# Kernel optimization log

Measured on AMD Instinct MI355X. Metric: run time of the kernel, lower is better.

Reference implementation:

```python
import jax, jax.numpy as jnp
import numpy as np

B, M, D, W = 4, 4096, 64, 128  # batch/heads, seq (m=n), head dim (k), nnz per row


def setup_inputs() -> dict:
    key = jax.random.key(0)
    kq, kk, kv, kc = jax.random.split(key, 4)
    q = jax.random.normal(kq, (B, M, D), dtype=jnp.float32)
    k = jax.random.normal(kk, (B, M, D), dtype=jnp.float32)
    v = jax.random.normal(kv, (B, M, D), dtype=jnp.float32)
    # CSR with uniform W nonzeros per row: row_offsets = arange(M+1)*W implicit,
    # column_indices flattened is [M*W]; stored here as [M, W].
    column_indices = jax.random.randint(kc, (M, W), 0, M).astype(jnp.int32)
    return {"q": q, "k": k, "v": v, "column_indices": column_indices}


def reference(q, k, v, column_indices):
    # SDDMM: logits[b,i,w] = <q[b,i,:], k[b, col[i,w], :]> at sparse positions only
    k_g = k[:, column_indices, :]                      # [B, M, W, D]
    logits = jnp.einsum('bmd,bmwd->bmw', q, k_g)       # sparse values per row
    # Sparse row-wise softmax (each CSR row has exactly W entries)
    weights = jax.nn.softmax(logits, axis=-1)          # [B, M, W]
    # SpMM: out[b,i,d] = sum_w weights[b,i,w] * v[b, col[i,w], d]
    v_g = v[:, column_indices, :]                      # [B, M, W, D]
    out = jnp.einsum('bmw,bmwd->bmd', weights, v_g)    # [B, M, D]
    return out
```

## Files before the change

### kernel.cpp

```cpp
#include <hip/hip_runtime.h>
#include <hip/hip_fp16.h>
#include <math.h>

constexpr int B = 4;
constexpr int M = 4096;
constexpr int D = 64;
constexpr int W = 128;
constexpr int NELEM = B * M * D;

typedef _Float16 h2_t __attribute__((ext_vector_type(2)));
typedef int      i4_t __attribute__((ext_vector_type(4)));

__global__ __launch_bounds__(256) void cvt_f32_f16_2(
    const float4* __restrict__ k, const float4* __restrict__ v,
    __half2* __restrict__ kh, __half2* __restrict__ vh, int n4) {
    int i = blockIdx.x * 256 + threadIdx.x;
    const float4* src;
    __half2* dst;
    if (i < n4) { src = k; dst = kh; }
    else        { src = v; dst = vh; i -= n4; if (i >= n4) return; }
    float4 f = src[i];
    dst[2 * i]     = __floats2half2_rn(f.x, f.y);
    dst[2 * i + 1] = __floats2half2_rn(f.z, f.w);
}

__global__ __launch_bounds__(256, 4) void sparse_attn_f16(
    const float* __restrict__ q,
    const __half* __restrict__ kh,
    const __half* __restrict__ vh,
    const int*   __restrict__ idx,
    float*       __restrict__ out)
{
    const int blk  = blockIdx.x;
    const int b    = blk & 3;
    const int mb   = (blk >> 2) * 4;
    const int t    = threadIdx.x;
    const int wave = t >> 6;
    const int lane = t & 63;
    const int ci   = lane & 7;
    const int r    = lane >> 3;
    const int m    = mb + wave;

    __shared__ int idx_s[4 * W];

    ((int2*)idx_s)[t] = ((const int2*)(idx + (size_t)mb * W))[t];

    const float* qrow = q + ((size_t)b * M + m) * D;
    const float4 qa = ((const float4*)qrow)[2 * ci];
    const float4 qb = ((const float4*)qrow)[2 * ci + 1];
    h2_t qh[4];
    qh[0] = (h2_t){(_Float16)qa.x, (_Float16)qa.y};
    qh[1] = (h2_t){(_Float16)qa.z, (_Float16)qa.w};
    qh[2] = (h2_t){(_Float16)qb.x, (_Float16)qb.y};
    qh[3] = (h2_t){(_Float16)qb.z, (_Float16)qb.w};

    __syncthreads();

    int voff[16];
    #pragma unroll
    for (int j = 0; j < 16; ++j)
        voff[j] = idx_s[wave * W + j * 8 + r] * (D * 2) + ci * 16;

    const char* kb = (const char*)(kh + (size_t)b * M * D);
    const char* vb = (const char*)(vh + (size_t)b * M * D);

    float larr[16];
    #pragma unroll
    for (int batch = 0; batch < 2; ++batch) {
        i4_t kreg[8];
        #pragma unroll
        for (int jj = 0; jj < 8; ++jj)
            kreg[jj] = __builtin_nontemporal_load(
                (const i4_t*)(kb + voff[batch * 8 + jj]));
        #pragma unroll
        for (int jj = 0; jj < 8; ++jj) {
            union { i4_t v; h2_t h[4]; } u;
            u.v = kreg[jj];
            float part = 0.f;
            part = __builtin_amdgcn_fdot2(u.h[0], qh[0], part, false);
            part = __builtin_amdgcn_fdot2(u.h[1], qh[1], part, false);
            part = __builtin_amdgcn_fdot2(u.h[2], qh[2], part, false);
            part = __builtin_amdgcn_fdot2(u.h[3], qh[3], part, false);
            part += __shfl_xor(part, 1);
            part += __shfl_xor(part, 2);
            part += __shfl_xor(part, 4);
            larr[batch * 8 + jj] = part;
        }
    }

    i4_t vreg0[8];
    #pragma unroll
    for (int jj = 0; jj < 8; ++jj)
        vreg0[jj] = __builtin_nontemporal_load((const i4_t*)(vb + voff[jj]));

    float mx = larr[0];
    #pragma unroll
    for (int j = 1; j < 16; ++j) mx = fmaxf(mx, larr[j]);
    mx = fmaxf(mx, __shfl_xor(mx, 8));
    mx = fmaxf(mx, __shfl_xor(mx, 16));
    mx = fmaxf(mx, __shfl_xor(mx, 32));

    float sum = 0.f;
    #pragma unroll
    for (int j = 0; j < 16; ++j) { larr[j] = __expf(larr[j] - mx); sum += larr[j]; }
    sum += __shfl_xor(sum, 8);
    sum += __shfl_xor(sum, 16);
    sum += __shfl_xor(sum, 32);
    const float inv = 1.0f / sum;

    float acc[8] = {0, 0, 0, 0, 0, 0, 0, 0};
    i4_t vreg1[8];
    #pragma unroll
    for (int jj = 0; jj < 8; ++jj)
        vreg1[jj] = __builtin_nontemporal_load((const i4_t*)(vb + voff[8 + jj]));

    #pragma unroll
    for (int jj = 0; jj < 8; ++jj) {
        const float p = larr[jj];
        union { i4_t v; h2_t h[4]; } u;
        u.v = vreg0[jj];
        #pragma unroll
        for (int c = 0; c < 4; ++c) {
            acc[2 * c]     += p * (float)u.h[c][0];
            acc[2 * c + 1] += p * (float)u.h[c][1];
        }
    }
    #pragma unroll
    for (int jj = 0; jj < 8; ++jj) {
        const float p = larr[8 + jj];
        union { i4_t v; h2_t h[4]; } u;
        u.v = vreg1[jj];
        #pragma unroll
        for (int c = 0; c < 4; ++c) {
            acc[2 * c]     += p * (float)u.h[c][0];
            acc[2 * c + 1] += p * (float)u.h[c][1];
        }
    }
    #pragma unroll
    for (int o = 8; o < 64; o <<= 1) {
        #pragma unroll
        for (int i = 0; i < 8; ++i) acc[i] += __shfl_xor(acc[i], o);
    }

    if (r == 0) {
        float4* orow = (float4*)(out + ((size_t)b * M + m) * D);
        orow[2 * ci]     = make_float4(acc[0] * inv, acc[1] * inv,
                                       acc[2] * inv, acc[3] * inv);
        orow[2 * ci + 1] = make_float4(acc[4] * inv, acc[5] * inv,
                                       acc[6] * inv, acc[7] * inv);
    }
}

__global__ __launch_bounds__(128) void sparse_attn_f32(
    const float* __restrict__ q,
    const float* __restrict__ k,
    const float* __restrict__ v,
    const int*   __restrict__ idx,
    float*       __restrict__ out)
{
    const int blk = blockIdx.x;
    const int b = blk & 3;
    const int m = blk >> 2;
    const int t = threadIdx.x;
    const int lane = t & 63;
    const int wave = t >> 6;
    const int ci = lane & 15;
    const int r  = lane >> 4;

    __shared__ int   idx_s[W];
    __shared__ float sc_s[W];
    __shared__ float red_s[4];
    __shared__ float4 opart_s[16];

    idx_s[t] = idx[m * W + t];
    const float4 qf = ((const float4*)(q + ((size_t)b * M + m) * D))[ci];
    __syncthreads();

    const float* kb = k + (size_t)b * M * D;
    const int wbase = wave * 64;

    #pragma unroll
    for (int j = 0; j < 16; ++j) {
        const int w = wbase + j * 4 + r;
        const float4 kv = ((const float4*)(kb + (size_t)idx_s[w] * D))[ci];
        float part = kv.x * qf.x + kv.y * qf.y + kv.z * qf.z + kv.w * qf.w;
        part += __shfl_xor(part, 1);
        part += __shfl_xor(part, 2);
        part += __shfl_xor(part, 4);
        part += __shfl_xor(part, 8);
        if (ci == 0) sc_s[w] = part;
    }
    __syncthreads();

    float logit = sc_s[t];
    float mx = logit;
    #pragma unroll
    for (int o = 1; o < 64; o <<= 1) mx = fmaxf(mx, __shfl_xor(mx, o));
    if (lane == 0) red_s[wave] = mx;
    __syncthreads();
    mx = fmaxf(red_s[0], red_s[1]);
    float e = __expf(logit - mx);
    float sm = e;
    #pragma unroll
    for (int o = 1; o < 64; o <<= 1) sm += __shfl_xor(sm, o);
    if (lane == 0) red_s[2 + wave] = sm;
    __syncthreads();
    const float inv_denom = 1.0f / (red_s[2] + red_s[3]);
    sc_s[t] = e * inv_denom;
    __syncthreads();

    const float* vb = v + (size_t)b * M * D;
    float4 acc = {0.f, 0.f, 0.f, 0.f};
    #pragma unroll
    for (int j = 0; j < 16; ++j) {
        const int w = wbase + j * 4 + r;
        const float p = sc_s[w];
        const float4 vv = ((const float4*)(vb + (size_t)idx_s[w] * D))[ci];
        acc.x += p * vv.x; acc.y += p * vv.y;
        acc.z += p * vv.z; acc.w += p * vv.w;
    }
    acc.x += __shfl_xor(acc.x, 16); acc.y += __shfl_xor(acc.y, 16);
    acc.z += __shfl_xor(acc.z, 16); acc.w += __shfl_xor(acc.w, 16);
    acc.x += __shfl_xor(acc.x, 32); acc.y += __shfl_xor(acc.y, 32);
    acc.z += __shfl_xor(acc.z, 32); acc.w += __shfl_xor(acc.w, 32);

    if (wave == 0 && r == 0) opart_s[ci] = acc;
    __syncthreads();
    if (wave == 1 && r == 0) {
        const float4 o0 = opart_s[ci];
        float4 res;
        res.x = o0.x + acc.x; res.y = o0.y + acc.y;
        res.z = o0.z + acc.z; res.w = o0.w + acc.w;
        ((float4*)(out + ((size_t)b * M + m) * D))[ci] = res;
    }
}

extern "C" void kernel_launch(void* const* d_in, const int* in_sizes, int n_in,
                              void* d_out, int out_size, void* d_ws, size_t ws_size,
                              hipStream_t stream) {
    const float* q = (const float*)d_in[0];
    const float* k = (const float*)d_in[1];
    const float* v = (const float*)d_in[2];
    const int* idx = (const int*)d_in[3];
    float* out = (float*)d_out;

    const size_t need = (size_t)2 * NELEM * sizeof(__half);
    if (ws_size >= need) {
        __half* kh = (__half*)d_ws;
        __half* vh = kh + NELEM;
        const int n4 = NELEM / 4;
        const int cblk = (2 * n4 + 255) / 256;
        cvt_f32_f16_2<<<cblk, 256, 0, stream>>>((const float4*)k, (const float4*)v,
                                                (__half2*)kh, (__half2*)vh, n4);
        sparse_attn_f16<<<B * M / 4, 256, 0, stream>>>(q, kh, vh, idx, out);
    } else {
        sparse_attn_f32<<<B * M, 128, 0, stream>>>(q, k, v, idx, out);
    }
}
```

Before: 93.72 us.

## Spill logits to LDS and shrink load batches to raise occupancy

The fp16 sparse attention kernel now writes logits and exp weights to shared memory instead of holding 16 logits and 16 V vectors in registers. K and V gathers are issued in smaller batches of 4, and launch bounds are raised to 8 blocks per CU to get more waves in flight for latency hiding. The cost is fewer outstanding loads per wave, extra LDS traffic and two extra block barriers. V loads also no longer overlap with the softmax.

```diff
diff --git a/kernel.cpp b/kernel.cpp
--- a/kernel.cpp
+++ b/kernel.cpp
@@ -24,7 +24,7 @@
     dst[2 * i + 1] = __floats2half2_rn(f.z, f.w);
 }
 
-__global__ __launch_bounds__(256, 4) void sparse_attn_f16(
+__global__ __launch_bounds__(256, 8) void sparse_attn_f16(
     const float* __restrict__ q,
     const __half* __restrict__ kh,
     const __half* __restrict__ vh,
@@ -41,7 +41,8 @@
     const int r    = lane >> 3;
     const int m    = mb + wave;
 
-    __shared__ int idx_s[4 * W];
+    __shared__ int   idx_s[4 * W];
+    __shared__ float sc_s[4 * W];
 
     ((int2*)idx_s)[t] = ((const int2*)(idx + (size_t)mb * W))[t];
 
@@ -56,24 +57,23 @@
 
     __syncthreads();
 
-    int voff[16];
-    #pragma unroll
-    for (int j = 0; j < 16; ++j)
-        voff[j] = idx_s[wave * W + j * 8 + r] * (D * 2) + ci * 16;
-
     const char* kb = (const char*)(kh + (size_t)b * M * D);
     const char* vb = (const char*)(vh + (size_t)b * M * D);
-
-    float larr[16];
-    #pragma unroll
-    for (int batch = 0; batch < 2; ++batch) {
-        i4_t kreg[8];
-        #pragma unroll
-        for (int jj = 0; jj < 8; ++jj)
-            kreg[jj] = __builtin_nontemporal_load(
-                (const i4_t*)(kb + voff[batch * 8 + jj]));
-        #pragma unroll
-        for (int jj = 0; jj < 8; ++jj) {
+    const int wrow = wave * W;
+
+    float mx = -1e30f;
+    #pragma unroll
+    for (int batch = 0; batch < 4; ++batch) {
+        int voff[4];
+        #pragma unroll
+        for (int jj = 0; jj < 4; ++jj)
+            voff[jj] = idx_s[wrow + (batch * 4 + jj) * 8 + r] * (D * 2) + ci * 16;
+        i4_t kreg[4];
+        #pragma unroll
+        for (int jj = 0; jj < 4; ++jj)
+            kreg[jj] = __builtin_nontemporal_load((const i4_t*)(kb + voff[jj]));
+        #pragma unroll
+        for (int jj = 0; jj < 4; ++jj) {
             union { i4_t v; h2_t h[4]; } u;
             u.v = kreg[jj];
             float part = 0.f;
@@ -84,56 +84,51 @@
             part += __shfl_xor(part, 1);
             part += __shfl_xor(part, 2);
             part += __shfl_xor(part, 4);
-            larr[batch * 8 + jj] = part;
+            if (ci == 0) sc_s[wrow + (batch * 4 + jj) * 8 + r] = part;
+            mx = fmaxf(mx, part);
         }
     }
-
-    i4_t vreg0[8];
-    #pragma unroll
-    for (int jj = 0; jj < 8; ++jj)
-        vreg0[jj] = __builtin_nontemporal_load((const i4_t*)(vb + voff[jj]));
-
-    float mx = larr[0];
-    #pragma unroll
-    for (int j = 1; j < 16; ++j) mx = fmaxf(mx, larr[j]);
     mx = fmaxf(mx, __shfl_xor(mx, 8));
     mx = fmaxf(mx, __shfl_xor(mx, 16));
     mx = fmaxf(mx, __shfl_xor(mx, 32));
 
-    float sum = 0.f;
-    #pragma unroll
-    for (int j = 0; j < 16; ++j) { larr[j] = __expf(larr[j] - mx); sum += larr[j]; }
-    sum += __shfl_xor(sum, 8);
-    sum += __shfl_xor(sum, 16);
-    sum += __shfl_xor(sum, 32);
+    __syncthreads();
+
+    float e0 = __expf(sc_s[wrow + lane] - mx);
+    float e1 = __expf(sc_s[wrow + 64 + lane] - mx);
+    float sum = e0 + e1;
+    #pragma unroll
+    for (int o = 1; o < 64; o <<= 1) sum += __shfl_xor(sum, o);
     const float inv = 1.0f / sum;
+    sc_s[wrow + lane]      = e0;
+    sc_s[wrow + 64 + lane] = e1;
+
+    __syncthreads();
 
     float acc[8] = {0, 0, 0, 0, 0, 0, 0, 0};
-    i4_t vreg1[8];
-    #pragma unroll
-    for (int jj = 0; jj < 8; ++jj)
-        vreg1[jj] = __builtin_nontemporal_load((const i4_t*)(vb + voff[8 + jj]));
-
-    #pragma unroll
-    for (int jj = 0; jj < 8; ++jj) {
-        const float p = larr[jj];
-        union { i4_t v; h2_t h[4]; } u;
-        u.v = vreg0[jj];
-        #pragma unroll
-        for (int c = 0; c < 4; ++c) {
-            acc[2 * c]     += p * (float)u.h[c][0];
-            acc[2 * c + 1] += p * (float)u.h[c][1];
+    #pragma unroll
+    for (int batch = 0; batch < 4; ++batch) {
+        int voff[4];
+        float p[4];
+        #pragma unroll
+        for (int jj = 0; jj < 4; ++jj) {
+            const int w = (batch * 4 + jj) * 8 + r;
+            voff[jj] = idx_s[wrow + w] * (D * 2) + ci * 16;
+            p[jj] = sc_s[wrow + w];
         }
-    }
-    #pragma unroll
-    for (int jj = 0; jj < 8; ++jj) {
-        const float p = larr[8 + jj];
-        union { i4_t v; h2_t h[4]; } u;
-        u.v = vreg1[jj];
-        #pragma unroll
-        for (int c = 0; c < 4; ++c) {
-            acc[2 * c]     += p * (float)u.h[c][0];
-            acc[2 * c + 1] += p * (float)u.h[c][1];
+        i4_t vreg[4];
+        #pragma unroll
+        for (int jj = 0; jj < 4; ++jj)
+            vreg[jj] = __builtin_nontemporal_load((const i4_t*)(vb + voff[jj]));
+        #pragma unroll
+        for (int jj = 0; jj < 4; ++jj) {
+            union { i4_t v; h2_t h[4]; } u;
+            u.v = vreg[jj];
+            #pragma unroll
+            for (int c = 0; c < 4; ++c) {
+                acc[2 * c]     += p[jj] * (float)u.h[c][0];
+                acc[2 * c + 1] += p[jj] * (float)u.h[c][1];
+            }
         }
     }
     #pragma unroll
```

Result: slower. 106.9 us (+14.1%).

## Interleave fp16 K and V rows and fuse SDDMM, softmax and SpMM in one pass

Applied to the files above, without the earlier changes.

The conversion kernel now writes K and V as fp16 into one interleaved 256-byte row per key: K in the first 128 bytes, V in the second. In the attention kernel, each 16-lane group fetches K and V for the same gathered index in a single contiguous load. Lanes 0-7 compute the dot product, and lanes 8-15 receive the logit by shuffle and accumulate exp(logit)*V directly. The separate max pass and the second V gather phase are gone, which shortens the dependent-latency chain and merges two scattered accesses per index into one. In exchange, half the lanes do wasted arithmetic. Dropping max subtraction also risks fp32 overflow if logits grow large.

```diff
diff --git a/kernel.cpp b/kernel.cpp
--- a/kernel.cpp
+++ b/kernel.cpp
@@ -7,27 +7,35 @@
 constexpr int D = 64;
 constexpr int W = 128;
 constexpr int NELEM = B * M * D;
+constexpr int ROWB  = 256;
 
 typedef _Float16 h2_t __attribute__((ext_vector_type(2)));
 typedef int      i4_t __attribute__((ext_vector_type(4)));
 
-__global__ __launch_bounds__(256) void cvt_f32_f16_2(
+__global__ __launch_bounds__(256) void cvt_interleave(
     const float4* __restrict__ k, const float4* __restrict__ v,
-    __half2* __restrict__ kh, __half2* __restrict__ vh, int n4) {
-    int i = blockIdx.x * 256 + threadIdx.x;
+    char* __restrict__ ws) {
+    const int half = B * M * 8;
+    int id = blockIdx.x * 256 + threadIdx.x;
     const float4* src;
-    __half2* dst;
-    if (i < n4) { src = k; dst = kh; }
-    else        { src = v; dst = vh; i -= n4; if (i >= n4) return; }
-    float4 f = src[i];
-    dst[2 * i]     = __floats2half2_rn(f.x, f.y);
-    dst[2 * i + 1] = __floats2half2_rn(f.z, f.w);
-}
-
-__global__ __launch_bounds__(256, 4) void sparse_attn_f16(
+    int base;
+    if (id < half) { src = k; base = 0; }
+    else           { src = v; base = 128; id -= half; if (id >= half) return; }
+    const int row = id >> 3;
+    const int cc  = id & 7;
+    float4 f0 = src[row * 16 + cc * 2];
+    float4 f1 = src[row * 16 + cc * 2 + 1];
+    union { __half2 h[4]; i4_t v4; } u;
+    u.h[0] = __floats2half2_rn(f0.x, f0.y);
+    u.h[1] = __floats2half2_rn(f0.z, f0.w);
+    u.h[2] = __floats2half2_rn(f1.x, f1.y);
+    u.h[3] = __floats2half2_rn(f1.z, f1.w);
+    *(i4_t*)(ws + (size_t)row * ROWB + base + cc * 16) = u.v4;
+}
+
+__global__ __launch_bounds__(256, 4) void sparse_attn_ilv(
     const float* __restrict__ q,
-    const __half* __restrict__ kh,
-    const __half* __restrict__ vh,
+    const char*  __restrict__ ws,
     const int*   __restrict__ idx,
     float*       __restrict__ out)
 {
@@ -37,17 +45,17 @@
     const int t    = threadIdx.x;
     const int wave = t >> 6;
     const int lane = t & 63;
-    const int ci   = lane & 7;
-    const int r    = lane >> 3;
+    const int rg   = lane >> 4;
+    const int c    = lane & 15;
+    const int kc   = c & 7;
     const int m    = mb + wave;
 
     __shared__ int idx_s[4 * W];
-
     ((int2*)idx_s)[t] = ((const int2*)(idx + (size_t)mb * W))[t];
 
     const float* qrow = q + ((size_t)b * M + m) * D;
-    const float4 qa = ((const float4*)qrow)[2 * ci];
-    const float4 qb = ((const float4*)qrow)[2 * ci + 1];
+    const float4 qa = ((const float4*)qrow)[2 * kc];
+    const float4 qb = ((const float4*)qrow)[2 * kc + 1];
     h2_t qh[4];
     qh[0] = (h2_t){(_Float16)qa.x, (_Float16)qa.y};
     qh[1] = (h2_t){(_Float16)qa.z, (_Float16)qa.w};
@@ -56,26 +64,26 @@
 
     __syncthreads();
 
-    int voff[16];
-    #pragma unroll
-    for (int j = 0; j < 16; ++j)
-        voff[j] = idx_s[wave * W + j * 8 + r] * (D * 2) + ci * 16;
-
-    const char* kb = (const char*)(kh + (size_t)b * M * D);
-    const char* vb = (const char*)(vh + (size_t)b * M * D);
-
-    float larr[16];
-    #pragma unroll
-    for (int batch = 0; batch < 2; ++batch) {
-        i4_t kreg[8];
+    const char* plane = ws + (size_t)b * M * ROWB;
+    const int wrow = wave * W;
+
+    float2 acc[4] = {{0,0},{0,0},{0,0},{0,0}};
+    float sum = 0.f;
+
+    #pragma unroll
+    for (int batch = 0; batch < 4; ++batch) {
+        int voff[8];
         #pragma unroll
         for (int jj = 0; jj < 8; ++jj)
-            kreg[jj] = __builtin_nontemporal_load(
-                (const i4_t*)(kb + voff[batch * 8 + jj]));
+            voff[jj] = idx_s[wrow + (batch * 8 + jj) * 4 + rg] * ROWB + c * 16;
+        i4_t reg[8];
+        #pragma unroll
+        for (int jj = 0; jj < 8; ++jj)
+            reg[jj] = __builtin_nontemporal_load((const i4_t*)(plane + voff[jj]));
         #pragma unroll
         for (int jj = 0; jj < 8; ++jj) {
             union { i4_t v; h2_t h[4]; } u;
-            u.v = kreg[jj];
+            u.v = reg[jj];
             float part = 0.f;
             part = __builtin_amdgcn_fdot2(u.h[0], qh[0], part, false);
             part = __builtin_amdgcn_fdot2(u.h[1], qh[1], part, false);
@@ -84,70 +92,39 @@
             part += __shfl_xor(part, 1);
             part += __shfl_xor(part, 2);
             part += __shfl_xor(part, 4);
-            larr[batch * 8 + jj] = part;
+            const float recv  = __shfl_xor(part, 8);
+            const float logit = (c < 8) ? part : recv;
+            const float e = __expf(logit);
+            sum += e;
+            float2 f0 = __half22float2(*(const __half2*)&u.h[0]);
+            float2 f1 = __half22float2(*(const __half2*)&u.h[1]);
+            float2 f2 = __half22float2(*(const __half2*)&u.h[2]);
+            float2 f3 = __half22float2(*(const __half2*)&u.h[3]);
+            acc[0].x += e * f0.x; acc[0].y += e * f0.y;
+            acc[1].x += e * f1.x; acc[1].y += e * f1.y;
+            acc[2].x += e * f2.x; acc[2].y += e * f2.y;
+            acc[3].x += e * f3.x; acc[3].y += e * f3.y;
         }
     }
 
-    i4_t vreg0[8];
-    #pragma unroll
-    for (int jj = 0; jj < 8; ++jj)
-        vreg0[jj] = __builtin_nontemporal_load((const i4_t*)(vb + voff[jj]));
-
-    float mx = larr[0];
-    #pragma unroll
-    for (int j = 1; j < 16; ++j) mx = fmaxf(mx, larr[j]);
-    mx = fmaxf(mx, __shfl_xor(mx, 8));
-    mx = fmaxf(mx, __shfl_xor(mx, 16));
-    mx = fmaxf(mx, __shfl_xor(mx, 32));
-
-    float sum = 0.f;
-    #pragma unroll
-    for (int j = 0; j < 16; ++j) { larr[j] = __expf(larr[j] - mx); sum += larr[j]; }
-    sum += __shfl_xor(sum, 8);
-    sum += __shfl_xor(sum, 16);
-    sum += __shfl_xor(sum, 32);
+    #pragma unroll
+    for (int o = 16; o < 64; o <<= 1) {
+        sum += __shfl_xor(sum, o);
+        #pragma unroll
+        for (int i = 0; i < 4; ++i) {
+            acc[i].x += __shfl_xor(acc[i].x, o);
+            acc[i].y += __shfl_xor(acc[i].y, o);
+        }
+    }
     const float inv = 1.0f / sum;
 
-    float acc[8] = {0, 0, 0, 0, 0, 0, 0, 0};
-    i4_t vreg1[8];
-    #pragma unroll
-    for (int jj = 0; jj < 8; ++jj)
-        vreg1[jj] = __builtin_nontemporal_load((const i4_t*)(vb + voff[8 + jj]));
-
-    #pragma unroll
-    for (int jj = 0; jj < 8; ++jj) {
-        const float p = larr[jj];
-        union { i4_t v; h2_t h[4]; } u;
-        u.v = vreg0[jj];
-        #pragma unroll
-        for (int c = 0; c < 4; ++c) {
-            acc[2 * c]     += p * (float)u.h[c][0];
-            acc[2 * c + 1] += p * (float)u.h[c][1];
-        }
-    }
-    #pragma unroll
-    for (int jj = 0; jj < 8; ++jj) {
-        const float p = larr[8 + jj];
-        union { i4_t v; h2_t h[4]; } u;
-        u.v = vreg1[jj];
-        #pragma unroll
-        for (int c = 0; c < 4; ++c) {
-            acc[2 * c]     += p * (float)u.h[c][0];
-            acc[2 * c + 1] += p * (float)u.h[c][1];
-        }
-    }
-    #pragma unroll
-    for (int o = 8; o < 64; o <<= 1) {
-        #pragma unroll
-        for (int i = 0; i < 8; ++i) acc[i] += __shfl_xor(acc[i], o);
-    }
-
-    if (r == 0) {
+    if (rg == 0 && c >= 8) {
         float4* orow = (float4*)(out + ((size_t)b * M + m) * D);
-        orow[2 * ci]     = make_float4(acc[0] * inv, acc[1] * inv,
-                                       acc[2] * inv, acc[3] * inv);
-        orow[2 * ci + 1] = make_float4(acc[4] * inv, acc[5] * inv,
-                                       acc[6] * inv, acc[7] * inv);
+        const int d4 = (c - 8) * 2;
+        orow[d4]     = make_float4(acc[0].x * inv, acc[0].y * inv,
+                                   acc[1].x * inv, acc[1].y * inv);
+        orow[d4 + 1] = make_float4(acc[2].x * inv, acc[2].y * inv,
+                                   acc[3].x * inv, acc[3].y * inv);
     }
 }
 
@@ -244,15 +221,13 @@
     const int* idx = (const int*)d_in[3];
     float* out = (float*)d_out;
 
-    const size_t need = (size_t)2 * NELEM * sizeof(__half);
+    const size_t need = (size_t)B * M * ROWB;
     if (ws_size >= need) {
-        __half* kh = (__half*)d_ws;
-        __half* vh = kh + NELEM;
-        const int n4 = NELEM / 4;
-        const int cblk = (2 * n4 + 255) / 256;
-        cvt_f32_f16_2<<<cblk, 256, 0, stream>>>((const float4*)k, (const float4*)v,
-                                                (__half2*)kh, (__half2*)vh, n4);
-        sparse_attn_f16<<<B * M / 4, 256, 0, stream>>>(q, kh, vh, idx, out);
+        char* ws = (char*)d_ws;
+        const int nthreads = 2 * B * M * 8;
+        cvt_interleave<<<(nthreads + 255) / 256, 256, 0, stream>>>(
+            (const float4*)k, (const float4*)v, ws);
+        sparse_attn_ilv<<<B * M / 4, 256, 0, stream>>>(q, ws, idx, out);
     } else {
         sparse_attn_f32<<<B * M, 128, 0, stream>>>(q, k, v, idx, out);
     }
```

Result: slower. 101.6 us (+8.4%).

## Split fp16 K/V rows into two 64-byte half-planes for gather

Applied to the files above, without the earlier changes.

The conversion kernel now writes K and V as fp16 into four separate planes, each holding one 32-element half of every row (64 bytes), with 256-byte padding between planes. The attention kernel sends lanes ci<4 to the first plane and ci>=4 to the second, so each gathered row is fetched as two 64-byte segments in different regions instead of one contiguous 128-byte row. This may change cache-line and channel distribution for the random gathers, and may help bank or channel conflicts, but each gather now touches two separate lines instead of one. The half-to-float conversion is also switched to __half22float2.

```diff
diff --git a/kernel.cpp b/kernel.cpp
--- a/kernel.cpp
+++ b/kernel.cpp
@@ -8,26 +8,41 @@
 constexpr int W = 128;
 constexpr int NELEM = B * M * D;
 
+constexpr size_t HP  = (size_t)B * M * 64;
+constexpr size_t K0O = 0;
+constexpr size_t K1O = HP + 256;
+constexpr size_t V0O = 2 * HP + 512;
+constexpr size_t V1O = 3 * HP + 768;
+constexpr size_t WS_NEED = 4 * HP + 768;
+
 typedef _Float16 h2_t __attribute__((ext_vector_type(2)));
 typedef int      i4_t __attribute__((ext_vector_type(4)));
 
-__global__ __launch_bounds__(256) void cvt_f32_f16_2(
+__global__ __launch_bounds__(256) void cvt_split(
     const float4* __restrict__ k, const float4* __restrict__ v,
-    __half2* __restrict__ kh, __half2* __restrict__ vh, int n4) {
-    int i = blockIdx.x * 256 + threadIdx.x;
-    const float4* src;
-    __half2* dst;
-    if (i < n4) { src = k; dst = kh; }
-    else        { src = v; dst = vh; i -= n4; if (i >= n4) return; }
-    float4 f = src[i];
-    dst[2 * i]     = __floats2half2_rn(f.x, f.y);
-    dst[2 * i + 1] = __floats2half2_rn(f.z, f.w);
+    char* __restrict__ ws) {
+    int id = blockIdx.x * 256 + threadIdx.x;
+    if (id >= 2 * B * M * 8) return;
+    const int tensor = id >> 17;
+    const int j      = id & 131071;
+    const int g      = j >> 3;
+    const int half   = (j >> 2) & 1;
+    const int chunk  = j & 3;
+    const float4* src = tensor ? v : k;
+    float4 f0 = src[g * 16 + half * 8 + chunk * 2];
+    float4 f1 = src[g * 16 + half * 8 + chunk * 2 + 1];
+    union { __half2 h[4]; i4_t v4; } u;
+    u.h[0] = __floats2half2_rn(f0.x, f0.y);
+    u.h[1] = __floats2half2_rn(f0.z, f0.w);
+    u.h[2] = __floats2half2_rn(f1.x, f1.y);
+    u.h[3] = __floats2half2_rn(f1.z, f1.w);
+    const size_t base = (tensor ? V0O : K0O) + (half ? (HP + 256) : 0);
+    *(i4_t*)(ws + base + (size_t)g * 64 + chunk * 16) = u.v4;
 }
 
 __global__ __launch_bounds__(256, 4) void sparse_attn_f16(
     const float* __restrict__ q,
-    const __half* __restrict__ kh,
-    const __half* __restrict__ vh,
+    const char*  __restrict__ ws,
     const int*   __restrict__ idx,
     float*       __restrict__ out)
 {
@@ -40,6 +55,7 @@
     const int ci   = lane & 7;
     const int r    = lane >> 3;
     const int m    = mb + wave;
+    const int chunk = ci & 3;
 
     __shared__ int idx_s[4 * W];
 
@@ -56,13 +72,14 @@
 
     __syncthreads();
 
+    const size_t boff = (size_t)b * M * 64;
+    const char* kb = ws + (ci >= 4 ? K1O : K0O) + boff;
+    const char* vb = ws + (ci >= 4 ? V1O : V0O) + boff;
+
     int voff[16];
     #pragma unroll
     for (int j = 0; j < 16; ++j)
-        voff[j] = idx_s[wave * W + j * 8 + r] * (D * 2) + ci * 16;
-
-    const char* kb = (const char*)(kh + (size_t)b * M * D);
-    const char* vb = (const char*)(vh + (size_t)b * M * D);
+        voff[j] = idx_s[wave * W + j * 8 + r] * 64 + chunk * 16;
 
     float larr[16];
     #pragma unroll
@@ -121,8 +138,9 @@
         u.v = vreg0[jj];
         #pragma unroll
         for (int c = 0; c < 4; ++c) {
-            acc[2 * c]     += p * (float)u.h[c][0];
-            acc[2 * c + 1] += p * (float)u.h[c][1];
+            float2 f = __half22float2(*(const __half2*)&u.h[c]);
+            acc[2 * c]     += p * f.x;
+            acc[2 * c + 1] += p * f.y;
         }
     }
     #pragma unroll
@@ -132,8 +150,9 @@
         u.v = vreg1[jj];
         #pragma unroll
         for (int c = 0; c < 4; ++c) {
-            acc[2 * c]     += p * (float)u.h[c][0];
-            acc[2 * c + 1] += p * (float)u.h[c][1];
+            float2 f = __half22float2(*(const __half2*)&u.h[c]);
+            acc[2 * c]     += p * f.x;
+            acc[2 * c + 1] += p * f.y;
         }
     }
     #pragma unroll
@@ -244,15 +263,12 @@
     const int* idx = (const int*)d_in[3];
     float* out = (float*)d_out;
 
-    const size_t need = (size_t)2 * NELEM * sizeof(__half);
-    if (ws_size >= need) {
-        __half* kh = (__half*)d_ws;
-        __half* vh = kh + NELEM;
-        const int n4 = NELEM / 4;
-        const int cblk = (2 * n4 + 255) / 256;
-        cvt_f32_f16_2<<<cblk, 256, 0, stream>>>((const float4*)k, (const float4*)v,
-                                                (__half2*)kh, (__half2*)vh, n4);
-        sparse_attn_f16<<<B * M / 4, 256, 0, stream>>>(q, kh, vh, idx, out);
+    if (ws_size >= WS_NEED) {
+        char* ws = (char*)d_ws;
+        const int nthreads = 2 * B * M * 8;
+        cvt_split<<<(nthreads + 255) / 256, 256, 0, stream>>>(
+            (const float4*)k, (const float4*)v, ws);
+        sparse_attn_f16<<<B * M / 4, 256, 0, stream>>>(q, ws, idx, out);
     } else {
         sparse_attn_f32<<<B * M, 128, 0, stream>>>(q, k, v, idx, out);
     }
```

Measured after the change: 105.2 us. 1.12x slower.
